# Performance work log

Measured on AMD Instinct MI355X. Metric: run time of the kernel, lower is better.

The kernel has to match this reference:

```python
import jax, jax.numpy as jnp
import numpy as np

T, H, I, E, TOPK = 1024, 1024, 2816, 16, 4


def setup_inputs() -> dict:
    key = jax.random.key(0)
    ks = jax.random.split(key, 5)
    s_h = 1.0 / np.sqrt(H)
    s_i = 1.0 / np.sqrt(I)
    return {
        "x": jax.random.normal(ks[0], (T, H), jnp.float32),
        "Wg": jax.random.normal(ks[1], (E, H), jnp.float32) * s_h,
        "gate_w": jax.random.normal(ks[2], (E, H, I), jnp.float32) * s_h,
        "up_w": jax.random.normal(ks[3], (E, H, I), jnp.float32) * s_h,
        "down_w": jax.random.normal(ks[4], (E, I, H), jnp.float32) * s_i,
        "top_k": TOPK,
    }


def reference(x, Wg, gate_w, up_w, down_w, top_k):
    # Router: softmax over expert logits, top-k, renormalize
    logits = x @ Wg.T                                   # [T, E]
    probs = jax.nn.softmax(logits, axis=-1)
    topk_w, topk_ids = jax.lax.top_k(probs, top_k)      # [T, K]
    topk_w = topk_w / jnp.sum(topk_w, axis=-1, keepdims=True)

    # Dense combine weights [T, E]: zero for unselected experts -> exact same
    # math as the per-token dispatch loop in the original module.
    n_tok = x.shape[0]
    combine = jnp.zeros((n_tok, Wg.shape[0]), x.dtype)
    combine = combine.at[jnp.arange(n_tok)[:, None], topk_ids].add(topk_w)

    # SwiGLU per expert, batched over the expert axis
    g = jax.nn.silu(jnp.einsum('th,ehi->eti', x, gate_w))  # [E, T, I]
    u = jnp.einsum('th,ehi->eti', x, up_w)                 # [E, T, I]
    y = jnp.einsum('eti,eih->eth', g * u, down_w)          # [E, T, H]

    # Weighted combine across experts
    return jnp.einsum('eth,te->th', y, combine)            # [T, H]
```

## Files before the change

### kernel.cpp

```cpp
#include <hip/hip_runtime.h>

static constexpr int cT = 1024;
static constexpr int cH = 1024;
static constexpr int cI = 2816;
static constexpr int cE = 16;
static constexpr int cK = 4;

typedef __attribute__((ext_vector_type(8))) short bf16x8;
typedef __attribute__((ext_vector_type(4))) float f32x4;
typedef __attribute__((ext_vector_type(2))) unsigned uint2v;
typedef __attribute__((ext_vector_type(4))) unsigned uint4v;

__device__ __forceinline__ unsigned f2bf(float f) {
  unsigned u = __float_as_uint(f);
  return (u + 0x7FFFu + ((u >> 16) & 1u)) >> 16;
}
__device__ __forceinline__ unsigned pack2(float lo, float hi) {
  return f2bf(lo) | (f2bf(hi) << 16);
}

__device__ __forceinline__ bf16x8 ld_bfrag(const unsigned* p) {
  union { uint2v d[2]; bf16x8 v; } r;
  r.d[0] = *(const uint2v*)p;
  r.d[1] = *(const uint2v*)(p + 2);
  return r.v;
}

__global__ __launch_bounds__(256) void xcast_kernel(
    const float* __restrict__ x, unsigned short* __restrict__ xb) {
  const int i = blockIdx.x * 256 + threadIdx.x;
  const float4* xv = (const float4*)x;
  const float4 a = xv[i * 2], b = xv[i * 2 + 1];
  uint4v o;
  o.x = pack2(a.x, a.y); o.y = pack2(a.z, a.w);
  o.z = pack2(b.x, b.y); o.w = pack2(b.z, b.w);
  ((uint4v*)xb)[i] = o;
}

__global__ __launch_bounds__(64) void router_kernel(
    const float* __restrict__ x, const float* __restrict__ Wg,
    int* __restrict__ topk_id, float* __restrict__ topk_w,
    int* __restrict__ counts) {
  const int t = blockIdx.x;
  const int l = threadIdx.x;

  float xa[16];
#pragma unroll
  for (int i = 0; i < 16; ++i) xa[i] = x[(size_t)t * cH + l + 64 * i];

  float lg[16];
#pragma unroll
  for (int e = 0; e < 16; ++e) {
    float s = 0.f;
#pragma unroll
    for (int i = 0; i < 16; ++i) s += xa[i] * Wg[(size_t)e * cH + l + 64 * i];
#pragma unroll
    for (int d = 1; d < 64; d <<= 1) s += __shfl_xor(s, d);
    lg[e] = s;
  }

  if (l == 0) {
    int ids[4]; float vals[4];
    unsigned taken = 0;
#pragma unroll
    for (int j = 0; j < 4; ++j) {
      float m = -1e30f; int mi = 0;
#pragma unroll
      for (int e = 0; e < 16; ++e) {
        bool better = !((taken >> e) & 1u) && lg[e] > m;
        if (better) { m = lg[e]; mi = e; }
      }
      taken |= 1u << mi; ids[j] = mi; vals[j] = m;
    }
    const float mx = vals[0];
    float s = 0.f;
#pragma unroll
    for (int j = 0; j < 4; ++j) { vals[j] = __expf(vals[j] - mx); s += vals[j]; }
    const float inv = 1.f / s;
#pragma unroll
    for (int j = 0; j < 4; ++j) {
      topk_id[t * 4 + j] = ids[j];
      topk_w[t * 4 + j] = vals[j] * inv;
      atomicAdd(&counts[ids[j]], 1);
    }
  }
}

__global__ void scan_kernel(const int* __restrict__ counts,
                            int* __restrict__ offsets) {
  if (threadIdx.x == 0 && blockIdx.x == 0) {
    int acc = 0;
    for (int e = 0; e < cE; ++e) { offsets[e] = acc; acc += counts[e]; }
    offsets[cE] = acc;
  }
}

__global__ __launch_bounds__(256) void scatter_kernel(
    const int* __restrict__ topk_id, const int* __restrict__ offsets,
    int* __restrict__ cursor, int* __restrict__ pair_token,
    int* __restrict__ pair_pos) {
  const int i = blockIdx.x * 256 + threadIdx.x;
  const int t = i >> 2;
  const int e = topk_id[i];
  const int pos = offsets[e] + atomicAdd(&cursor[e], 1);
  pair_token[pos] = t;
  pair_pos[i] = pos;
}

__global__ __launch_bounds__(512, 4) void gateup_kernel(
    const unsigned short* __restrict__ xb, const float* __restrict__ gw,
    const float* __restrict__ uw, const int* __restrict__ offsets,
    const int* __restrict__ pair_token, unsigned short* __restrict__ act) {
  const int e = blockIdx.y;
  const int off = offsets[e];
  const int n_e = offsets[e + 1] - off;
  if (n_e <= 0) return;
  const int nb = blockIdx.x * 32;
  const int tid = threadIdx.x, l = tid & 63, wid = tid >> 6;
  const int q = l & 15, h16 = l >> 4;

  __shared__ unsigned sB[2][2][1088];
  __shared__ int tokl[384];

  const int tm = tid >> 8, tt = tid & 255;
  const int rq = tt >> 3, cg = tt & 7;
  const float* wsrc = (tm ? uw : gw) + (size_t)e * cH * cI + nb + cg * 4;

  float4 s0[2];

#define GU_LD(KT)                                                             \
  _Pragma("unroll")                                                           \
  for (int i = 0; i < 2; ++i)                                                 \
    s0[i] = *(const float4*)(wsrc + (size_t)((KT) * 64 + rq * 2 + i) * cI);

#define GU_PACK(BUF)                                                          \
  _Pragma("unroll")                                                           \
  for (int i = 0; i < 4; ++i)                                                 \
    sB[BUF][tm][(cg * 4 + i) * 34 + rq] = pack2(s0[0][i], s0[1][i]);

#define GU_MFMA(CUR, KT)                                                      \
  _Pragma("unroll")                                                           \
  for (int ks = 0; ks < 2; ++ks) {                                            \
    bf16x8 af[3];                                                             \
    _Pragma("unroll")                                                         \
    for (int mf = 0; mf < 3; ++mf)                                            \
      af[mf] = *(const bf16x8*)(ap[mf] + (KT) * 64 + ks * 32);                \
    _Pragma("unroll")                                                         \
    for (int mt = 0; mt < 2; ++mt) {                                          \
      _Pragma("unroll")                                                       \
      for (int ni = 0; ni < 2; ++ni) {                                        \
        const bf16x8 b =                                                      \
            ld_bfrag(&sB[CUR][mt][(q + 16 * ni) * 34 + h16 * 4 + 16 * ks]);   \
        _Pragma("unroll")                                                     \
        for (int mf = 0; mf < 3; ++mf)                                        \
          acc[mt][mf][ni] = __builtin_amdgcn_mfma_f32_16x16x32_bf16(          \
              af[mf], b, acc[mt][mf][ni], 0, 0, 0);                           \
      }                                                                       \
    }                                                                         \
  }

  for (int m0 = 0; m0 < n_e; m0 += 384) {
    if (tid < 384) tokl[tid] = pair_token[off + min(m0 + tid, n_e - 1)];

    f32x4 acc[2][3][2];
#pragma unroll
    for (int mt = 0; mt < 2; ++mt)
#pragma unroll
      for (int mf = 0; mf < 3; ++mf)
#pragma unroll
        for (int ni = 0; ni < 2; ++ni)
          acc[mt][mf][ni] = (f32x4){0.f, 0.f, 0.f, 0.f};

    GU_LD(0)
    GU_PACK(0)
    GU_LD(1)
    __syncthreads();

    const unsigned short* ap[3];
#pragma unroll
    for (int mf = 0; mf < 3; ++mf)
      ap[mf] = xb + (size_t)tokl[wid * 48 + mf * 16 + q] * cH + h16 * 8;

    for (int kt = 0; kt < 16; ++kt) {
      const int cur = kt & 1;
      if (kt + 1 < 16) { GU_PACK(1 - cur) }
      if (kt + 2 < 16) { GU_LD(kt + 2) }
      GU_MFMA(cur, kt)
      if (kt + 1 < 16) __syncthreads();
    }

#pragma unroll
    for (int mf = 0; mf < 3; ++mf)
#pragma unroll
      for (int j = 0; j < 4; ++j) {
        const int er = m0 + wid * 48 + mf * 16 + h16 * 4 + j;
        if (er < n_e) {
#pragma unroll
          for (int ni = 0; ni < 2; ++ni) {
            const float g = acc[0][mf][ni][j];
            const float u = acc[1][mf][ni][j];
            const float v = (g / (1.f + __expf(-g))) * u;
            act[(size_t)(off + er) * cI + nb + ni * 16 + q] =
                (unsigned short)f2bf(v);
          }
        }
      }
  }
#undef GU_LD
#undef GU_PACK
#undef GU_MFMA
}

__global__ __launch_bounds__(512, 4) void down_kernel(
    const unsigned short* __restrict__ act, const float* __restrict__ dw,
    const int* __restrict__ offsets, float* __restrict__ yp) {
  const int e = blockIdx.y;
  const int off = offsets[e];
  const int n_e = offsets[e + 1] - off;
  if (n_e <= 0) return;
  const int nb = blockIdx.x * 32;
  const int tid = threadIdx.x, l = tid & 63, wid = tid >> 6;
  const int q = l & 15, h16 = l >> 4;
  constexpr int NT = cI / 64;

  __shared__ unsigned sB[2][1088];

  const int rq = tid >> 4, cg = tid & 15;
  const float* dsrc = dw + (size_t)e * cI * cH + nb + cg * 2;

  float2 s0[2];

#define DN_LD(KT)                                                             \
  _Pragma("unroll")                                                           \
  for (int i = 0; i < 2; ++i)                                                 \
    s0[i] = *(const float2*)(dsrc + (size_t)((KT) * 64 + rq * 2 + i) * cH);

#define DN_PACK(BUF)                                                          \
  sB[BUF][(cg * 2) * 34 + rq] = pack2(s0[0].x, s0[1].x);                      \
  sB[BUF][(cg * 2 + 1) * 34 + rq] = pack2(s0[0].y, s0[1].y);

#define DN_MFMA(CUR, KT)                                                      \
  _Pragma("unroll")                                                           \
  for (int ks = 0; ks < 2; ++ks) {                                            \
    bf16x8 af[3];                                                             \
    _Pragma("unroll")                                                         \
    for (int mf = 0; mf < 3; ++mf)                                            \
      af[mf] = *(const bf16x8*)(ap[mf] + (KT) * 64 + ks * 32);                \
    _Pragma("unroll")                                                         \
    for (int ni = 0; ni < 2; ++ni) {                                          \
      const bf16x8 b =                                                        \
          ld_bfrag(&sB[CUR][(q + 16 * ni) * 34 + h16 * 4 + 16 * ks]);         \
      _Pragma("unroll")                                                       \
      for (int mf = 0; mf < 3; ++mf)                                          \
        acc[mf][ni] = __builtin_amdgcn_mfma_f32_16x16x32_bf16(                \
            af[mf], b, acc[mf][ni], 0, 0, 0);                                 \
    }                                                                         \
  }

  for (int m0 = 0; m0 < n_e; m0 += 384) {
    const unsigned short* ap[3];
#pragma unroll
    for (int mf = 0; mf < 3; ++mf) {
      const int r = min(m0 + wid * 48 + mf * 16 + q, n_e - 1);
      ap[mf] = act + (size_t)(off + r) * cI + h16 * 8;
    }

    f32x4 acc[3][2];
#pragma unroll
    for (int mf = 0; mf < 3; ++mf)
#pragma unroll
      for (int ni = 0; ni < 2; ++ni) acc[mf][ni] = (f32x4){0.f, 0.f, 0.f, 0.f};

    DN_LD(0)
    DN_PACK(0)
    DN_LD(1)
    __syncthreads();

    for (int kt = 0; kt < NT; ++kt) {
      const int cur = kt & 1;
      if (kt + 1 < NT) { DN_PACK(1 - cur) }
      if (kt + 2 < NT) { DN_LD(kt + 2) }
      DN_MFMA(cur, kt)
      if (kt + 1 < NT) __syncthreads();
    }

#pragma unroll
    for (int mf = 0; mf < 3; ++mf)
#pragma unroll
      for (int j = 0; j < 4; ++j) {
        const int er = m0 + wid * 48 + mf * 16 + h16 * 4 + j;
        if (er < n_e) {
#pragma unroll
          for (int ni = 0; ni < 2; ++ni)
            yp[(size_t)(off + er) * cH + nb + ni * 16 + q] = acc[mf][ni][j];
        }
      }

    if (m0 + 384 < n_e) __syncthreads();
  }
#undef DN_LD
#undef DN_PACK
#undef DN_MFMA
}

__global__ __launch_bounds__(256) void combine_kernel(
    const float* __restrict__ yp, const int* __restrict__ pair_pos,
    const float* __restrict__ topk_w, float* __restrict__ out) {
  const int t = blockIdx.x;
  const int cb = threadIdx.x * 4;
  float4 s = make_float4(0.f, 0.f, 0.f, 0.f);
#pragma unroll
  for (int j = 0; j < 4; ++j) {
    const int pos = pair_pos[t * 4 + j];
    const float wj = topk_w[t * 4 + j];
    const float4 v = *(const float4*)(yp + (size_t)pos * cH + cb);
    s.x += wj * v.x; s.y += wj * v.y; s.z += wj * v.z; s.w += wj * v.w;
  }
  *(float4*)(out + (size_t)t * cH + cb) = s;
}

extern "C" void kernel_launch(void* const* d_in, const int* in_sizes, int n_in,
                              void* d_out, int out_size, void* d_ws,
                              size_t ws_size, hipStream_t stream) {
  (void)in_sizes; (void)n_in; (void)out_size; (void)ws_size;
  const float* x = (const float*)d_in[0];
  const float* Wg = (const float*)d_in[1];
  const float* gw = (const float*)d_in[2];
  const float* uw = (const float*)d_in[3];
  const float* dw = (const float*)d_in[4];
  float* out = (float*)d_out;

  char* ws = (char*)d_ws;
  int* counts     = (int*)(ws + 0);
  int* cursor     = (int*)(ws + 64);
  int* offsets    = (int*)(ws + 128);
  int* topk_id    = (int*)(ws + 256);
  float* topk_w   = (float*)(ws + 256 + 16384);
  int* pair_token = (int*)(ws + 256 + 32768);
  int* pair_pos   = (int*)(ws + 256 + 49152);
  unsigned short* act = (unsigned short*)(ws + 65792);
  unsigned short* xb  = (unsigned short*)(ws + 65792 + (size_t)4096 * 2816 * 2);
  float* yp = (float*)(ws + 65792 + (size_t)4096 * 2816 * 2 + (size_t)cT * cH * 2);

  (void)hipMemsetAsync(ws, 0, 128, stream);

  xcast_kernel<<<cT * cH / (256 * 8), 256, 0, stream>>>(x, xb);
  router_kernel<<<cT, 64, 0, stream>>>(x, Wg, topk_id, topk_w, counts);
  scan_kernel<<<1, 1, 0, stream>>>(counts, offsets);
  scatter_kernel<<<cT * cK / 256, 256, 0, stream>>>(topk_id, offsets, cursor,
                                                    pair_token, pair_pos);
  gateup_kernel<<<dim3(cI / 32, cE), 512, 0, stream>>>(xb, gw, uw, offsets,
                                                       pair_token, act);
  down_kernel<<<dim3(cH / 32, cE), 512, 0, stream>>>(act, dw, offsets, yp);
  combine_kernel<<<cT, 256, 0, stream>>>(yp, pair_pos, topk_w, out);
}
```

Baseline: 445.0 us.

## Unroll GEMM k-loops by two with explicit register double-buffering and lighter barriers

Both the gate/up and down kernels now unroll the k-tile loop by two and alternate two register staging sets for weight loads. A-fragment global loads are issued at the start of each tile, and sched_barrier pins the load order. The __syncthreads calls are replaced by an inline s_waitcnt lgkmcnt(0) plus s_barrier that does not wait for outstanding global loads, so prefetches stay in flight across barriers. The goal is better overlap of global memory latency with MFMA work, at the cost of more registers and fragile hand-written synchronisation; the trailing sync between m0 tiles in down_kernel is also removed.

```diff
diff --git a/kernel.cpp b/kernel.cpp
--- a/kernel.cpp
+++ b/kernel.cpp
@@ -17,6 +17,10 @@
 }
 __device__ __forceinline__ unsigned pack2(float lo, float hi) {
   return f2bf(lo) | (f2bf(hi) << 16);
+}
+
+__device__ __forceinline__ void bar_nodrain() {
+  asm volatile("s_waitcnt lgkmcnt(0)\n\ts_barrier" ::: "memory");
 }
 
 __device__ __forceinline__ bf16x8 ld_bfrag(const unsigned* p) {
@@ -126,25 +130,29 @@
   const int rq = tt >> 3, cg = tt & 7;
   const float* wsrc = (tm ? uw : gw) + (size_t)e * cH * cI + nb + cg * 4;
 
-  float4 s0[2];
-
-#define GU_LD(KT)                                                             \
+  float4 s0[2], s1[2];
+  bf16x8 af[3][2];
+
+#define GU_LD(S, KT)                                                          \
   _Pragma("unroll")                                                           \
   for (int i = 0; i < 2; ++i)                                                 \
-    s0[i] = *(const float4*)(wsrc + (size_t)((KT) * 64 + rq * 2 + i) * cI);
-
-#define GU_PACK(BUF)                                                          \
+    S[i] = *(const float4*)(wsrc + (size_t)((KT) * 64 + rq * 2 + i) * cI);
+
+#define GU_PACK(BUF, S)                                                       \
   _Pragma("unroll")                                                           \
   for (int i = 0; i < 4; ++i)                                                 \
-    sB[BUF][tm][(cg * 4 + i) * 34 + rq] = pack2(s0[0][i], s0[1][i]);
-
-#define GU_MFMA(CUR, KT)                                                      \
+    sB[BUF][tm][(cg * 4 + i) * 34 + rq] = pack2(S[0][i], S[1][i]);
+
+#define GU_LDA(KT)                                                            \
+  _Pragma("unroll")                                                           \
+  for (int mf = 0; mf < 3; ++mf) {                                            \
+    af[mf][0] = *(const bf16x8*)(ap[mf] + (KT) * 64);                         \
+    af[mf][1] = *(const bf16x8*)(ap[mf] + (KT) * 64 + 32);                    \
+  }
+
+#define GU_MFMA(CUR)                                                          \
   _Pragma("unroll")                                                           \
   for (int ks = 0; ks < 2; ++ks) {                                            \
-    bf16x8 af[3];                                                             \
-    _Pragma("unroll")                                                         \
-    for (int mf = 0; mf < 3; ++mf)                                            \
-      af[mf] = *(const bf16x8*)(ap[mf] + (KT) * 64 + ks * 32);                \
     _Pragma("unroll")                                                         \
     for (int mt = 0; mt < 2; ++mt) {                                          \
       _Pragma("unroll")                                                       \
@@ -154,7 +162,7 @@
         _Pragma("unroll")                                                     \
         for (int mf = 0; mf < 3; ++mf)                                        \
           acc[mt][mf][ni] = __builtin_amdgcn_mfma_f32_16x16x32_bf16(          \
-              af[mf], b, acc[mt][mf][ni], 0, 0, 0);                           \
+              af[mf][ks], b, acc[mt][mf][ni], 0, 0, 0);                       \
       }                                                                       \
     }                                                                         \
   }
@@ -171,22 +179,31 @@
         for (int ni = 0; ni < 2; ++ni)
           acc[mt][mf][ni] = (f32x4){0.f, 0.f, 0.f, 0.f};
 
-    GU_LD(0)
-    GU_PACK(0)
-    GU_LD(1)
-    __syncthreads();
+    GU_LD(s1, 0)
+    GU_PACK(0, s1)
+    GU_LD(s0, 1)
+    bar_nodrain();
 
     const unsigned short* ap[3];
 #pragma unroll
     for (int mf = 0; mf < 3; ++mf)
       ap[mf] = xb + (size_t)tokl[wid * 48 + mf * 16 + q] * cH + h16 * 8;
 
-    for (int kt = 0; kt < 16; ++kt) {
-      const int cur = kt & 1;
-      if (kt + 1 < 16) { GU_PACK(1 - cur) }
-      if (kt + 2 < 16) { GU_LD(kt + 2) }
-      GU_MFMA(cur, kt)
-      if (kt + 1 < 16) __syncthreads();
+    for (int kt = 0; kt < 16; kt += 2) {
+      GU_LDA(kt)
+      __builtin_amdgcn_sched_barrier(0);
+      if (kt + 2 < 16) { GU_LD(s1, kt + 2) }
+      __builtin_amdgcn_sched_barrier(0);
+      GU_PACK(1, s0)
+      GU_MFMA(0)
+      bar_nodrain();
+      GU_LDA(kt + 1)
+      __builtin_amdgcn_sched_barrier(0);
+      if (kt + 3 < 16) { GU_LD(s0, kt + 3) }
+      __builtin_amdgcn_sched_barrier(0);
+      if (kt + 2 < 16) { GU_PACK(0, s1) }
+      GU_MFMA(1)
+      if (kt + 2 < 16) bar_nodrain();
     }
 
 #pragma unroll
@@ -208,6 +225,7 @@
   }
 #undef GU_LD
 #undef GU_PACK
+#undef GU_LDA
 #undef GU_MFMA
 }
 
@@ -228,24 +246,28 @@
   const int rq = tid >> 4, cg = tid & 15;
   const float* dsrc = dw + (size_t)e * cI * cH + nb + cg * 2;
 
-  float2 s0[2];
-
-#define DN_LD(KT)                                                             \
+  float2 s0[2], s1[2];
+  bf16x8 af[3][2];
+
+#define DN_LD(S, KT)                                                          \
   _Pragma("unroll")                                                           \
   for (int i = 0; i < 2; ++i)                                                 \
-    s0[i] = *(const float2*)(dsrc + (size_t)((KT) * 64 + rq * 2 + i) * cH);
-
-#define DN_PACK(BUF)                                                          \
-  sB[BUF][(cg * 2) * 34 + rq] = pack2(s0[0].x, s0[1].x);                      \
-  sB[BUF][(cg * 2 + 1) * 34 + rq] = pack2(s0[0].y, s0[1].y);
-
-#define DN_MFMA(CUR, KT)                                                      \
+    S[i] = *(const float2*)(dsrc + (size_t)((KT) * 64 + rq * 2 + i) * cH);
+
+#define DN_PACK(BUF, S)                                                       \
+  sB[BUF][(cg * 2) * 34 + rq] = pack2(S[0].x, S[1].x);                        \
+  sB[BUF][(cg * 2 + 1) * 34 + rq] = pack2(S[0].y, S[1].y);
+
+#define DN_LDA(KT)                                                            \
+  _Pragma("unroll")                                                           \
+  for (int mf = 0; mf < 3; ++mf) {                                            \
+    af[mf][0] = *(const bf16x8*)(ap[mf] + (KT) * 64);                         \
+    af[mf][1] = *(const bf16x8*)(ap[mf] + (KT) * 64 + 32);                    \
+  }
+
+#define DN_MFMA(CUR)                                                          \
   _Pragma("unroll")                                                           \
   for (int ks = 0; ks < 2; ++ks) {                                            \
-    bf16x8 af[3];                                                             \
-    _Pragma("unroll")                                                         \
-    for (int mf = 0; mf < 3; ++mf)                                            \
-      af[mf] = *(const bf16x8*)(ap[mf] + (KT) * 64 + ks * 32);                \
     _Pragma("unroll")                                                         \
     for (int ni = 0; ni < 2; ++ni) {                                          \
       const bf16x8 b =                                                        \
@@ -253,7 +275,7 @@
       _Pragma("unroll")                                                       \
       for (int mf = 0; mf < 3; ++mf)                                          \
         acc[mf][ni] = __builtin_amdgcn_mfma_f32_16x16x32_bf16(                \
-            af[mf], b, acc[mf][ni], 0, 0, 0);                                 \
+            af[mf][ks], b, acc[mf][ni], 0, 0, 0);                             \
     }                                                                         \
   }
 
@@ -271,17 +293,26 @@
 #pragma unroll
       for (int ni = 0; ni < 2; ++ni) acc[mf][ni] = (f32x4){0.f, 0.f, 0.f, 0.f};
 
-    DN_LD(0)
-    DN_PACK(0)
-    DN_LD(1)
-    __syncthreads();
-
-    for (int kt = 0; kt < NT; ++kt) {
-      const int cur = kt & 1;
-      if (kt + 1 < NT) { DN_PACK(1 - cur) }
-      if (kt + 2 < NT) { DN_LD(kt + 2) }
-      DN_MFMA(cur, kt)
-      if (kt + 1 < NT) __syncthreads();
+    DN_LD(s1, 0)
+    DN_PACK(0, s1)
+    DN_LD(s0, 1)
+    bar_nodrain();
+
+    for (int kt = 0; kt < NT; kt += 2) {
+      DN_LDA(kt)
+      __builtin_amdgcn_sched_barrier(0);
+      if (kt + 2 < NT) { DN_LD(s1, kt + 2) }
+      __builtin_amdgcn_sched_barrier(0);
+      DN_PACK(1, s0)
+      DN_MFMA(0)
+      bar_nodrain();
+      DN_LDA(kt + 1)
+      __builtin_amdgcn_sched_barrier(0);
+      if (kt + 3 < NT) { DN_LD(s0, kt + 3) }
+      __builtin_amdgcn_sched_barrier(0);
+      if (kt + 2 < NT) { DN_PACK(0, s1) }
+      DN_MFMA(1)
+      if (kt + 2 < NT) bar_nodrain();
     }
 
 #pragma unroll
@@ -295,11 +326,10 @@
             yp[(size_t)(off + er) * cH + nb + ni * 16 + q] = acc[mf][ni][j];
         }
       }
-
-    if (m0 + 384 < n_e) __syncthreads();
   }
 #undef DN_LD
 #undef DN_PACK
+#undef DN_LDA
 #undef DN_MFMA
 }
 
```

Result: slower. 459.5 us (+3.2%).
